# Kernel tuning notes

Hardware: AMD Instinct MI355X
Metric: run time of the kernel (lower is better)

## Reference

```python
import jax, jax.numpy as jnp
import numpy as np


def setup_inputs() -> dict:
    key = jax.random.key(0)
    k0, k1, k2, k3 = jax.random.split(key, 4)
    B, S, D, E = 8, 4096, 1024, 3
    tokens = jax.random.normal(k0, (B, S, D), dtype=jnp.float32)
    # nn.Linear weights are [out_features, in_features]; kaiming-uniform-like scale
    scale = 1.0 / np.sqrt(D)
    Wq = jax.random.uniform(k1, (E, D), jnp.float32, -scale, scale)
    Wk = jax.random.uniform(k2, (E, D), jnp.float32, -scale, scale)
    Wv = jax.random.uniform(k3, (E, D), jnp.float32, -scale, scale)
    return {"tokens": tokens, "Wq": Wq, "Wk": Wk, "Wv": Wv}


def reference(tokens, Wq, Wk, Wv):
    # q, k, v: [B, S, E]   (E = num_experts = 3)
    q = jnp.einsum("bsd,ed->bse", tokens, Wq)
    k = jnp.einsum("bsd,ed->bse", tokens, Wk)
    v = jnp.einsum("bsd,ed->bse", tokens, Wv)
    # outer product attention: [B, S, E, E]
    attn = q[..., :, None] * k[..., None, :]
    attn = jax.nn.softmax(attn, axis=-1)
    # attn @ v: [B, S, E]
    logits = jnp.einsum("bsef,bsf->bse", attn, v)
    weights = jax.nn.softmax(logits, axis=-1)
    return weights
```

## Files before the change

### kernel.cpp

```cpp
#include <hip/hip_runtime.h>
#include <hip/hip_bf16.h>

typedef float f4 __attribute__((ext_vector_type(4)));
typedef float f32x4 __attribute__((ext_vector_type(4)));
typedef short s16x8 __attribute__((ext_vector_type(8)));


#define TPB 32

__device__ __forceinline__ s16x8 pack8(f4 a, f4 b) {
  union { s16x8 v; __hip_bfloat162 h[4]; } u;
  u.h[0] = __float22bfloat162_rn({a.x, a.y});
  u.h[1] = __float22bfloat162_rn({a.z, a.w});
  u.h[2] = __float22bfloat162_rn({b.x, b.y});
  u.h[3] = __float22bfloat162_rn({b.z, b.w});
  return u.v;
}

__global__ __launch_bounds__(256)
void moa_mfma3(const float* __restrict__ tok,
               const float* __restrict__ Wq,
               const float* __restrict__ Wk,
               const float* __restrict__ Wv,
               float* __restrict__ out) {
  __shared__ float clds[4 * 512];
  const int tid  = threadIdx.x;
  const int wv   = tid >> 6;
  const int lane = tid & 63;
  const int n    = lane & 15;
  const int kg   = lane >> 4;
  const int kq   = wv * 256;

  const float* wrow = (n < 3) ? (Wq + n * 1024)
                    : (n < 6) ? (Wk + (n - 3) * 1024)
                    : (n < 9) ? (Wv + (n - 6) * 1024) : Wq;
  const bool wvalid = (n < 9);
  s16x8 bfrag[8];
#pragma unroll
  for (int s = 0; s < 8; ++s) {
    const float* p = wrow + kq + s * 32 + kg * 8;
    f4 wa = wvalid ? *(const f4*)p       : (f4)0.0f;
    f4 wb = wvalid ? *(const f4*)(p + 4) : (f4)0.0f;
    bfrag[s] = pack8(wa, wb);
  }

  const int T0 = blockIdx.x * TPB;
  const float* ap0 = tok + (size_t)(T0 + n) * 1024 + kq + kg * 8;
  const float* ap1 = ap0 + 16 * 1024;

  f32x4 acc0 = {0.f, 0.f, 0.f, 0.f}, acc1 = {0.f, 0.f, 0.f, 0.f};

  f4 r0[4][2], r1[4][2];
#pragma unroll
  for (int s = 0; s < 3; ++s) {
    r0[s][0] = *(const f4*)(ap0 + s * 32);
    r0[s][1] = *(const f4*)(ap0 + s * 32 + 4);
    r1[s][0] = *(const f4*)(ap1 + s * 32);
    r1[s][1] = *(const f4*)(ap1 + s * 32 + 4);
  }

#pragma unroll
  for (int s = 0; s < 8; ++s) {
    const int cs = s & 3, ns = (s + 3) & 3;
    if (s < 5) {
      r0[ns][0] = *(const f4*)(ap0 + (s + 3) * 32);
      r0[ns][1] = *(const f4*)(ap0 + (s + 3) * 32 + 4);
      r1[ns][0] = *(const f4*)(ap1 + (s + 3) * 32);
      r1[ns][1] = *(const f4*)(ap1 + (s + 3) * 32 + 4);
    }
    s16x8 a0 = pack8(r0[cs][0], r0[cs][1]);
    s16x8 a1 = pack8(r1[cs][0], r1[cs][1]);
    acc0 = __builtin_amdgcn_mfma_f32_16x16x32_bf16(a0, bfrag[s], acc0, 0, 0, 0);
    acc1 = __builtin_amdgcn_mfma_f32_16x16x32_bf16(a1, bfrag[s], acc1, 0, 0, 0);
  }

#pragma unroll
  for (int i = 0; i < 4; ++i) {
    const int row = kg * 4 + i;
    clds[wv * 512 + row * 16 + n]        = acc0[i];
    clds[wv * 512 + (16 + row) * 16 + n] = acc1[i];
  }
  __syncthreads();

  if (tid < TPB) {
    float r[9];
#pragma unroll
    for (int j = 0; j < 9; ++j)
      r[j] = (clds[tid * 16 + j] + clds[512 + tid * 16 + j]) +
             (clds[1024 + tid * 16 + j] + clds[1536 + tid * 16 + j]);
    float lg[3];
#pragma unroll
    for (int e = 0; e < 3; ++e) {
      float e0 = __expf(r[e] * r[3]);
      float e1 = __expf(r[e] * r[4]);
      float e2 = __expf(r[e] * r[5]);
      float den = (e0 + e1) + e2;
      float num = e0 * r[6] + e1 * r[7] + e2 * r[8];
      lg[e] = num * __builtin_amdgcn_rcpf(den);
    }
    float u0 = __expf(lg[0]);
    float u1 = __expf(lg[1]);
    float u2 = __expf(lg[2]);
    float rs = __builtin_amdgcn_rcpf((u0 + u1) + u2);
    float* op = out + (size_t)(T0 + tid) * 3;
    op[0] = u0 * rs;
    op[1] = u1 * rs;
    op[2] = u2 * rs;
  }
}

extern "C" void kernel_launch(void* const* d_in, const int* in_sizes, int n_in,
                              void* d_out, int out_size, void* d_ws, size_t ws_size,
                              hipStream_t stream) {
  const float* tok = (const float*)d_in[0];
  const float* Wq  = (const float*)d_in[1];
  const float* Wk  = (const float*)d_in[2];
  const float* Wv  = (const float*)d_in[3];
  float* out = (float*)d_out;

  const int n_tokens = in_sizes[0] / 1024;
  const int blocks   = n_tokens / TPB;

  hipLaunchKernelGGL(moa_mfma3, dim3(blocks), dim3(256), 0, stream,
                     tok, Wq, Wk, Wv, out);
}
```

Before: 28.14 us.

## Split K across eight waves with 16-token blocks and stream weights per step

Each block now handles 16 tokens using 512 threads. Eight waves each cover a 128-wide K slice, where before four waves each covered 256 wide and handled two 16-token tiles. Weights are no longer preloaded into registers up front; they are loaded and packed each step inside a double-buffered loop. The aim is more blocks and waves in flight to cover the latency of the memory-bound token stream. The cost is a longer 8-way reduction in LDS and weight loads repeated across twice as many blocks.

```diff
diff --git a/kernel.cpp b/kernel.cpp
--- a/kernel.cpp
+++ b/kernel.cpp
@@ -6,7 +6,7 @@
 typedef short s16x8 __attribute__((ext_vector_type(8)));
 
 
-#define TPB 32
+#define TPB 16
 
 __device__ __forceinline__ s16x8 pack8(f4 a, f4 b) {
   union { s16x8 v; __hip_bfloat162 h[4]; } u;
@@ -17,77 +17,68 @@
   return u.v;
 }
 
-__global__ __launch_bounds__(256)
-void moa_mfma3(const float* __restrict__ tok,
-               const float* __restrict__ Wq,
-               const float* __restrict__ Wk,
-               const float* __restrict__ Wv,
-               float* __restrict__ out) {
-  __shared__ float clds[4 * 512];
+__global__ __launch_bounds__(512)
+void moa_k8(const float* __restrict__ tok,
+            const float* __restrict__ Wq,
+            const float* __restrict__ Wk,
+            const float* __restrict__ Wv,
+            float* __restrict__ out) {
+  __shared__ float clds[8 * 256];
   const int tid  = threadIdx.x;
   const int wv   = tid >> 6;
   const int lane = tid & 63;
   const int n    = lane & 15;
   const int kg   = lane >> 4;
-  const int kq   = wv * 256;
+  const int kb   = wv * 128;
 
+  const int T0 = blockIdx.x * TPB;
+  const float* ap = tok + (size_t)(T0 + n) * 1024 + kb + kg * 8;
   const float* wrow = (n < 3) ? (Wq + n * 1024)
                     : (n < 6) ? (Wk + (n - 3) * 1024)
                     : (n < 9) ? (Wv + (n - 6) * 1024) : Wq;
   const bool wvalid = (n < 9);
-  s16x8 bfrag[8];
-#pragma unroll
-  for (int s = 0; s < 8; ++s) {
-    const float* p = wrow + kq + s * 32 + kg * 8;
-    f4 wa = wvalid ? *(const f4*)p       : (f4)0.0f;
-    f4 wb = wvalid ? *(const f4*)(p + 4) : (f4)0.0f;
-    bfrag[s] = pack8(wa, wb);
-  }
+  const float* bp = wrow + kb + kg * 8;
 
-  const int T0 = blockIdx.x * TPB;
-  const float* ap0 = tok + (size_t)(T0 + n) * 1024 + kq + kg * 8;
-  const float* ap1 = ap0 + 16 * 1024;
+  f32x4 acc = {0.f, 0.f, 0.f, 0.f};
 
-  f32x4 acc0 = {0.f, 0.f, 0.f, 0.f}, acc1 = {0.f, 0.f, 0.f, 0.f};
-
-  f4 r0[4][2], r1[4][2];
-#pragma unroll
-  for (int s = 0; s < 3; ++s) {
-    r0[s][0] = *(const f4*)(ap0 + s * 32);
-    r0[s][1] = *(const f4*)(ap0 + s * 32 + 4);
-    r1[s][0] = *(const f4*)(ap1 + s * 32);
-    r1[s][1] = *(const f4*)(ap1 + s * 32 + 4);
-  }
+  f4 A[2][2], B[2][2];
+  A[0][0] = *(const f4*)(ap);
+  A[0][1] = *(const f4*)(ap + 4);
+  B[0][0] = *(const f4*)(bp);
+  B[0][1] = *(const f4*)(bp + 4);
 
 #pragma unroll
-  for (int s = 0; s < 8; ++s) {
-    const int cs = s & 3, ns = (s + 3) & 3;
-    if (s < 5) {
-      r0[ns][0] = *(const f4*)(ap0 + (s + 3) * 32);
-      r0[ns][1] = *(const f4*)(ap0 + (s + 3) * 32 + 4);
-      r1[ns][0] = *(const f4*)(ap1 + (s + 3) * 32);
-      r1[ns][1] = *(const f4*)(ap1 + (s + 3) * 32 + 4);
+  for (int s = 0; s < 4; ++s) {
+    const int cs = s & 1, ns = cs ^ 1;
+    if (s < 3) {
+      A[ns][0] = *(const f4*)(ap + (s + 1) * 32);
+      A[ns][1] = *(const f4*)(ap + (s + 1) * 32 + 4);
+      B[ns][0] = *(const f4*)(bp + (s + 1) * 32);
+      B[ns][1] = *(const f4*)(bp + (s + 1) * 32 + 4);
     }
-    s16x8 a0 = pack8(r0[cs][0], r0[cs][1]);
-    s16x8 a1 = pack8(r1[cs][0], r1[cs][1]);
-    acc0 = __builtin_amdgcn_mfma_f32_16x16x32_bf16(a0, bfrag[s], acc0, 0, 0, 0);
-    acc1 = __builtin_amdgcn_mfma_f32_16x16x32_bf16(a1, bfrag[s], acc1, 0, 0, 0);
+    s16x8 a = pack8(A[cs][0], A[cs][1]);
+    f4 b0 = wvalid ? B[cs][0] : (f4)0.0f;
+    f4 b1 = wvalid ? B[cs][1] : (f4)0.0f;
+    s16x8 b = pack8(b0, b1);
+    acc = __builtin_amdgcn_mfma_f32_16x16x32_bf16(a, b, acc, 0, 0, 0);
   }
 
 #pragma unroll
   for (int i = 0; i < 4; ++i) {
     const int row = kg * 4 + i;
-    clds[wv * 512 + row * 16 + n]        = acc0[i];
-    clds[wv * 512 + (16 + row) * 16 + n] = acc1[i];
+    clds[wv * 256 + row * 16 + n] = acc[i];
   }
   __syncthreads();
 
   if (tid < TPB) {
     float r[9];
 #pragma unroll
-    for (int j = 0; j < 9; ++j)
-      r[j] = (clds[tid * 16 + j] + clds[512 + tid * 16 + j]) +
-             (clds[1024 + tid * 16 + j] + clds[1536 + tid * 16 + j]);
+    for (int j = 0; j < 9; ++j) {
+      float v = 0.0f;
+#pragma unroll
+      for (int w8 = 0; w8 < 8; ++w8) v += clds[w8 * 256 + tid * 16 + j];
+      r[j] = v;
+    }
     float lg[3];
 #pragma unroll
     for (int e = 0; e < 3; ++e) {
@@ -121,6 +112,6 @@
   const int n_tokens = in_sizes[0] / 1024;
   const int blocks   = n_tokens / TPB;
 
-  hipLaunchKernelGGL(moa_mfma3, dim3(blocks), dim3(256), 0, stream,
+  hipLaunchKernelGGL(moa_k8, dim3(blocks), dim3(512), 0, stream,
                      tok, Wq, Wk, Wv, out);
 }
```

Measured after the change: 33.74 us. 19.9% more time.
